# Kernel tuning notes

Hardware: AMD Instinct MI355X
Metric: run time of the kernel (lower is better)

Reference implementation:

```python
import jax, jax.numpy as jnp
import numpy as np

N_USER = 100000
N_ITEM = 50000
N = N_USER + N_ITEM
N_EDGES = 1200000
D = 64
NEG_SLOPE = 0.01  # torch leaky_relu default
EPS = 1e-12       # torch F.normalize default


def setup_inputs() -> dict:
    key = jax.random.key(0)
    ks = jax.random.split(key, 9)
    user_emb = jax.random.normal(ks[0], (N_USER, D), dtype=jnp.float32) * 0.1
    item_emb = jax.random.normal(ks[1], (N_ITEM, D), dtype=jnp.float32) * 0.1
    edge_row = jax.random.randint(ks[2], (N_EDGES,), 0, N, dtype=jnp.int32)
    edge_col = jax.random.randint(ks[3], (N_EDGES,), 0, N, dtype=jnp.int32)
    edge_val = jax.random.uniform(ks[4], (N_EDGES,), dtype=jnp.float32)
    Wf = jax.random.normal(ks[5], (3, D, D), dtype=jnp.float32) * (1.0 / np.sqrt(D))
    bf = jnp.zeros((3, D), dtype=jnp.float32)
    Wb = jax.random.normal(ks[6], (3, D, D), dtype=jnp.float32) * (1.0 / np.sqrt(D))
    bb = jnp.zeros((3, D), dtype=jnp.float32)
    return {"user_emb": user_emb, "item_emb": item_emb,
            "edge_row": edge_row, "edge_col": edge_col, "edge_val": edge_val,
            "Wf": Wf, "bf": bf, "Wb": Wb, "bb": bb}


def _spmm_plus_eye(edge_row, edge_col, edge_val, E):
    # (H + I) @ E : gather source features, scale, segment-sum into rows, add E
    msgs = edge_val[:, None] * E[edge_col]          # [n_edges, D]
    agg = jax.ops.segment_sum(msgs, edge_row, num_segments=N)
    return agg + E


def reference(user_emb, item_emb, edge_row, edge_col, edge_val, Wf, bf, Wb, bb):
    E_l = jnp.concatenate([user_emb, item_emb], axis=0)  # [N, D]
    all_emb = [E_l]
    for i in range(3):
        front = _spmm_plus_eye(edge_row, edge_col, edge_val, E_l)
        front_cal = jax.nn.leaky_relu(front @ Wf[i].T + bf[i], NEG_SLOPE)
        back = jax.nn.leaky_relu((E_l * front) @ Wb[i].T + bb[i], NEG_SLOPE)
        E_l = front_cal + back  # dropout p=0.5 treated as eval-mode identity
        norm = jnp.maximum(jnp.linalg.norm(E_l, axis=1, keepdims=True), EPS)
        all_emb.append(E_l / norm)
    all_emb = jnp.concatenate(all_emb, axis=1)  # [N, 4*D]
    return all_emb[:N_USER], all_emb[N_USER:]
```

## Files before the change

kernel.cpp:

```cpp
#include <hip/hip_runtime.h>
#include <hip/hip_bf16.h>
#include <stdint.h>

#define N_USER 100000
#define N_ITEM 50000
#define NTOT   150000
#define NEDGE  1200000
#define D      64
#define OUTD   256
#define NEG    0.01f
#define NBLK   586
#define LSTR   65

typedef __attribute__((ext_vector_type(8))) short short8;
typedef __attribute__((ext_vector_type(4))) float f32x4;

__device__ inline ushort f2bf(float x) {
    uint32_t u = __float_as_uint(x);
    u += 0x7fffu + ((u >> 16) & 1u);
    return (ushort)(u >> 16);
}
__device__ inline void split2(float x, ushort& h, ushort& l) {
    ushort hh = f2bf(x);
    float hf = __uint_as_float(((uint32_t)hh) << 16);
    h = hh;
    l = f2bf(x - hf);
}
__device__ inline void split8(const float* p, short8& h8, short8& l8) {
    float4 v0 = *(const float4*)p;
    float4 v1 = *(const float4*)(p + 4);
    float vv[8] = {v0.x, v0.y, v0.z, v0.w, v1.x, v1.y, v1.z, v1.w};
    #pragma unroll
    for (int e = 0; e < 8; e++) {
        ushort h, l;
        split2(vv[e], h, l);
        h8[e] = (short)h; l8[e] = (short)l;
    }
}

__global__ void k_init(const float* __restrict__ ue, const float* __restrict__ ie,
                       float* __restrict__ E, float* __restrict__ out) {
    int t = blockIdx.x * blockDim.x + threadIdx.x;
    if (t >= NTOT * 16) return;
    int r = t >> 4, q = t & 15;
    const float* src = (r < N_USER) ? (ue + (size_t)r * D)
                                    : (ie + (size_t)(r - N_USER) * D);
    float4 v = *(const float4*)(src + q * 4);
    *(float4*)(E + (size_t)r * D + q * 4) = v;
    *(float4*)(out + (size_t)r * OUTD + q * 4) = v;
}

__global__ void k_hist(const int* __restrict__ row, int* __restrict__ cnt) {
    int e = blockIdx.x * blockDim.x + threadIdx.x;
    if (e < NEDGE) atomicAdd(&cnt[row[e]], 1);
}

__global__ void k_scan_a(const int* __restrict__ cnt, int* __restrict__ part) {
    __shared__ int s[4];
    int i = blockIdx.x * 256 + threadIdx.x;
    int v = (i < NTOT) ? cnt[i] : 0;
    for (int off = 32; off; off >>= 1) v += __shfl_down(v, off, 64);
    if ((threadIdx.x & 63) == 0) s[threadIdx.x >> 6] = v;
    __syncthreads();
    if (threadIdx.x == 0) part[blockIdx.x] = s[0] + s[1] + s[2] + s[3];
}

__global__ void k_scan_b(int* __restrict__ part) {
    __shared__ int s[1024];
    int t = threadIdx.x;
    int v = (t < NBLK) ? part[t] : 0;
    s[t] = v;
    __syncthreads();
    for (int off = 1; off < 1024; off <<= 1) {
        int x = (t >= off) ? s[t - off] : 0;
        __syncthreads();
        s[t] += x;
        __syncthreads();
    }
    if (t < NBLK) part[t] = s[t] - v;
}

__global__ void k_scan_c(const int* __restrict__ cnt, const int* __restrict__ part,
                         int* __restrict__ offs, int* __restrict__ cur) {
    __shared__ int ws[4];
    int i = blockIdx.x * 256 + threadIdx.x;
    int v = (i < NTOT) ? cnt[i] : 0;
    int lane = threadIdx.x & 63, w = threadIdx.x >> 6;
    int x = v;
    for (int o = 1; o < 64; o <<= 1) {
        int y = __shfl_up(x, o, 64);
        if (lane >= o) x += y;
    }
    if (lane == 63) ws[w] = x;
    __syncthreads();
    int base = part[blockIdx.x];
    for (int k = 0; k < w; k++) base += ws[k];
    int excl = base + x - v;
    if (i < NTOT) { offs[i] = excl; cur[i] = excl; }
    if (i == 0) offs[NTOT] = NEDGE;
}

__global__ void k_scatter(const int* __restrict__ row, const int* __restrict__ col,
                          const float* __restrict__ val, int* __restrict__ cur,
                          int2* __restrict__ ce) {
    int e = blockIdx.x * blockDim.x + threadIdx.x;
    if (e >= NEDGE) return;
    int r = row[e];
    int p = atomicAdd(&cur[r], 1);
    int2 u;
    u.x = col[e];
    u.y = __float_as_int(val[e]);
    ce[p] = u;
}

__global__ void k_spmm(const float* __restrict__ E, const int* __restrict__ offs,
                       const int2* __restrict__ ce, float* __restrict__ front) {
    int r = blockIdx.x * (blockDim.x >> 6) + (threadIdx.x >> 6);
    int d = threadIdx.x & 63;
    if (r >= NTOT) return;
    int s = offs[r], e = offs[r + 1];
    float acc = E[(size_t)r * D + d];
    float a0 = 0.f, a1 = 0.f, a2 = 0.f, a3 = 0.f;
    int p = s;
    for (; p + 4 <= e; p += 4) {
        int2 c0 = ce[p + 0];
        int2 c1 = ce[p + 1];
        int2 c2 = ce[p + 2];
        int2 c3 = ce[p + 3];
        float x0 = E[(size_t)c0.x * D + d];
        float x1 = E[(size_t)c1.x * D + d];
        float x2 = E[(size_t)c2.x * D + d];
        float x3 = E[(size_t)c3.x * D + d];
        a0 = fmaf(__int_as_float(c0.y), x0, a0);
        a1 = fmaf(__int_as_float(c1.y), x1, a1);
        a2 = fmaf(__int_as_float(c2.y), x2, a2);
        a3 = fmaf(__int_as_float(c3.y), x3, a3);
    }
    for (; p < e; ++p) {
        int2 c = ce[p];
        acc = fmaf(__int_as_float(c.y), E[(size_t)c.x * D + d], acc);
    }
    acc += (a0 + a1) + (a2 + a3);
    front[(size_t)r * D + d] = acc;
}

__global__ __launch_bounds__(256) void k_rowmv(
    const float* __restrict__ front, float* __restrict__ E,
    const float* __restrict__ Wf, const float* __restrict__ bfv,
    const float* __restrict__ Wb, const float* __restrict__ bbv,
    float* __restrict__ out, int chunk) {
    __shared__ float sf[16 * LSTR];
    __shared__ float sg[16 * LSTR];
    __shared__ float nrm[16][4];

    int t  = threadIdx.x;
    int r0 = blockIdx.x * 16;

    {
        int row = t >> 4, km = (t & 15) * 4;
        const float* fp = front + (size_t)(r0 + row) * D + km;
        const float* ep = E     + (size_t)(r0 + row) * D + km;
        float4 a = *(const float4*)fp;
        float4 b = *(const float4*)ep;
        *(float4*)(sf + row * LSTR + km) = a;
        float4 gv;
        gv.x = a.x * b.x; gv.y = a.y * b.y; gv.z = a.z * b.z; gv.w = a.w * b.w;
        *(float4*)(sg + row * LSTR + km) = gv;
    }

    int lane = t & 63;
    int w    = t >> 6;
    int cl   = lane & 15;
    int kg   = lane >> 4;

    int col = w * 16 + cl;

    short8 wfh0, wfl0, wbh0, wbl0, wfh1, wfl1, wbh1, wbl1;
    split8(Wf + (size_t)col * D +  0 + kg * 8, wfh0, wfl0);
    split8(Wb + (size_t)col * D +  0 + kg * 8, wbh0, wbl0);
    split8(Wf + (size_t)col * D + 32 + kg * 8, wfh1, wfl1);
    split8(Wb + (size_t)col * D + 32 + kg * 8, wbh1, wbl1);
    float bF = bfv[col], bB = bbv[col];

    __syncthreads();

    f32x4 accF = {0.f, 0.f, 0.f, 0.f};
    f32x4 accB = {0.f, 0.f, 0.f, 0.f};
    {
        short8 fh, fl, gh, gl;
        split8(sf + cl * LSTR +  0 + kg * 8, fh, fl);
        split8(sg + cl * LSTR +  0 + kg * 8, gh, gl);
        accF = __builtin_amdgcn_mfma_f32_16x16x32_bf16(fh, wfh0, accF, 0, 0, 0);
        accB = __builtin_amdgcn_mfma_f32_16x16x32_bf16(gh, wbh0, accB, 0, 0, 0);
        accF = __builtin_amdgcn_mfma_f32_16x16x32_bf16(fl, wfh0, accF, 0, 0, 0);
        accB = __builtin_amdgcn_mfma_f32_16x16x32_bf16(gl, wbh0, accB, 0, 0, 0);
        accF = __builtin_amdgcn_mfma_f32_16x16x32_bf16(fh, wfl0, accF, 0, 0, 0);
        accB = __builtin_amdgcn_mfma_f32_16x16x32_bf16(gh, wbl0, accB, 0, 0, 0);
        split8(sf + cl * LSTR + 32 + kg * 8, fh, fl);
        split8(sg + cl * LSTR + 32 + kg * 8, gh, gl);
        accF = __builtin_amdgcn_mfma_f32_16x16x32_bf16(fh, wfh1, accF, 0, 0, 0);
        accB = __builtin_amdgcn_mfma_f32_16x16x32_bf16(gh, wbh1, accB, 0, 0, 0);
        accF = __builtin_amdgcn_mfma_f32_16x16x32_bf16(fl, wfh1, accF, 0, 0, 0);
        accB = __builtin_amdgcn_mfma_f32_16x16x32_bf16(gl, wbh1, accB, 0, 0, 0);
        accF = __builtin_amdgcn_mfma_f32_16x16x32_bf16(fh, wfl1, accF, 0, 0, 0);
        accB = __builtin_amdgcn_mfma_f32_16x16x32_bf16(gh, wbl1, accB, 0, 0, 0);
    }

    float e4[4], p4[4];
    #pragma unroll
    for (int rg = 0; rg < 4; rg++) {
        float aF = accF[rg] + bF;
        float aB = accB[rg] + bB;
        float vF = (aF > 0.f) ? aF : NEG * aF;
        float vB = (aB > 0.f) ? aB : NEG * aB;
        float e = vF + vB;
        e4[rg] = e;
        float p = e * e;
        p += __shfl_xor(p, 1, 64);
        p += __shfl_xor(p, 2, 64);
        p += __shfl_xor(p, 4, 64);
        p += __shfl_xor(p, 8, 64);
        p4[rg] = p;
    }
    if (cl == 0) {
        #pragma unroll
        for (int rg = 0; rg < 4; rg++) nrm[kg * 4 + rg][w] = p4[rg];
    }
    __syncthreads();
    #pragma unroll
    for (int rg = 0; rg < 4; rg++) {
        int row = kg * 4 + rg;
        float4 nv = *(const float4*)&nrm[row][0];
        float nsq = (nv.x + nv.y) + (nv.z + nv.w);
        float inv = 1.0f / fmaxf(sqrtf(nsq), 1e-12f);
        E[(size_t)(r0 + row) * D + col] = e4[rg];
        out[(size_t)(r0 + row) * OUTD + (size_t)chunk * D + col] = e4[rg] * inv;
    }
}

extern "C" void kernel_launch(void* const* d_in, const int* in_sizes, int n_in,
                              void* d_out, int out_size, void* d_ws, size_t ws_size,
                              hipStream_t stream) {
    const float* ue   = (const float*)d_in[0];
    const float* ie   = (const float*)d_in[1];
    const int*   erow = (const int*)d_in[2];
    const int*   ecol = (const int*)d_in[3];
    const float* eval = (const float*)d_in[4];
    const float* Wf   = (const float*)d_in[5];
    const float* bfv  = (const float*)d_in[6];
    const float* Wb   = (const float*)d_in[7];
    const float* bbv  = (const float*)d_in[8];
    float* out = (float*)d_out;

    float* E     = (float*)d_ws;
    float* front = E + (size_t)NTOT * D;
    float* invn  = front + (size_t)NTOT * D;
    int*   cnt   = (int*)(invn + NTOT);
    int*   offs  = cnt + NTOT;
    int*   cur   = offs + NTOT + 1;
    int*   part  = cur + NTOT;
    int2*  ce    = (int2*)(part + 1024);

    hipMemsetAsync(cnt, 0, NTOT * sizeof(int), stream);
    k_init<<<(NTOT * 16 + 255) / 256, 256, 0, stream>>>(ue, ie, E, out);
    k_hist<<<(NEDGE + 255) / 256, 256, 0, stream>>>(erow, cnt);
    k_scan_a<<<NBLK, 256, 0, stream>>>(cnt, part);
    k_scan_b<<<1, 1024, 0, stream>>>(part);
    k_scan_c<<<NBLK, 256, 0, stream>>>(cnt, part, offs, cur);
    k_scatter<<<(NEDGE + 255) / 256, 256, 0, stream>>>(erow, ecol, eval, cur, ce);

    for (int i = 0; i < 3; i++) {
        k_spmm<<<(NTOT + 3) / 4, 256, 0, stream>>>(E, offs, ce, front);
        k_rowmv<<<NTOT / 16, 256, 0, stream>>>(
            front, E, Wf + (size_t)i * D * D, bfv + (size_t)i * D,
            Wb + (size_t)i * D * D, bbv + (size_t)i * D, out, i + 1);
    }
}
```

Baseline: 700.7 us.

## Fuse SpMM into per-layer dense kernel with ping-pong E buffers

The separate SpMM and row-matmul kernels are merged into one per-layer kernel. Each block gathers neighbor rows for its 16 rows, with 16 lanes per row loading float4 chunks, and writes front and E*front straight into shared memory, so the front buffer no longer round-trips through global memory. E is double-buffered so one layer can read the old embeddings while writing the new ones, and the init and histogram kernels are merged into one launch. The trade-off is less parallelism in the gather: 16 threads per row instead of 64, with float4 loads, and 16 rows per block share one load-imbalance profile.

```diff
diff --git a/kernel.cpp b/kernel.cpp
--- a/kernel.cpp
+++ b/kernel.cpp
@@ -11,6 +11,7 @@
 #define NEG    0.01f
 #define NBLK   586
 #define LSTR   65
+#define INITBLK 9375
 
 typedef __attribute__((ext_vector_type(8))) short short8;
 typedef __attribute__((ext_vector_type(4))) float f32x4;
@@ -38,21 +39,21 @@
     }
 }
 
-__global__ void k_init(const float* __restrict__ ue, const float* __restrict__ ie,
-                       float* __restrict__ E, float* __restrict__ out) {
-    int t = blockIdx.x * blockDim.x + threadIdx.x;
-    if (t >= NTOT * 16) return;
-    int r = t >> 4, q = t & 15;
-    const float* src = (r < N_USER) ? (ue + (size_t)r * D)
-                                    : (ie + (size_t)(r - N_USER) * D);
-    float4 v = *(const float4*)(src + q * 4);
-    *(float4*)(E + (size_t)r * D + q * 4) = v;
-    *(float4*)(out + (size_t)r * OUTD + q * 4) = v;
-}
-
-__global__ void k_hist(const int* __restrict__ row, int* __restrict__ cnt) {
-    int e = blockIdx.x * blockDim.x + threadIdx.x;
-    if (e < NEDGE) atomicAdd(&cnt[row[e]], 1);
+__global__ void k_init_hist(const float* __restrict__ ue, const float* __restrict__ ie,
+                            float* __restrict__ E, float* __restrict__ out,
+                            const int* __restrict__ row, int* __restrict__ cnt) {
+    if (blockIdx.x < INITBLK) {
+        int t = blockIdx.x * 256 + threadIdx.x;
+        int r = t >> 4, q = t & 15;
+        const float* src = (r < N_USER) ? (ue + (size_t)r * D)
+                                        : (ie + (size_t)(r - N_USER) * D);
+        float4 v = *(const float4*)(src + q * 4);
+        *(float4*)(E + (size_t)r * D + q * 4) = v;
+        *(float4*)(out + (size_t)r * OUTD + q * 4) = v;
+    } else {
+        int e = (blockIdx.x - INITBLK) * 256 + threadIdx.x;
+        if (e < NEDGE) atomicAdd(&cnt[row[e]], 1);
+    }
 }
 
 __global__ void k_scan_a(const int* __restrict__ cnt, int* __restrict__ part) {
@@ -113,39 +114,9 @@
     ce[p] = u;
 }
 
-__global__ void k_spmm(const float* __restrict__ E, const int* __restrict__ offs,
-                       const int2* __restrict__ ce, float* __restrict__ front) {
-    int r = blockIdx.x * (blockDim.x >> 6) + (threadIdx.x >> 6);
-    int d = threadIdx.x & 63;
-    if (r >= NTOT) return;
-    int s = offs[r], e = offs[r + 1];
-    float acc = E[(size_t)r * D + d];
-    float a0 = 0.f, a1 = 0.f, a2 = 0.f, a3 = 0.f;
-    int p = s;
-    for (; p + 4 <= e; p += 4) {
-        int2 c0 = ce[p + 0];
-        int2 c1 = ce[p + 1];
-        int2 c2 = ce[p + 2];
-        int2 c3 = ce[p + 3];
-        float x0 = E[(size_t)c0.x * D + d];
-        float x1 = E[(size_t)c1.x * D + d];
-        float x2 = E[(size_t)c2.x * D + d];
-        float x3 = E[(size_t)c3.x * D + d];
-        a0 = fmaf(__int_as_float(c0.y), x0, a0);
-        a1 = fmaf(__int_as_float(c1.y), x1, a1);
-        a2 = fmaf(__int_as_float(c2.y), x2, a2);
-        a3 = fmaf(__int_as_float(c3.y), x3, a3);
-    }
-    for (; p < e; ++p) {
-        int2 c = ce[p];
-        acc = fmaf(__int_as_float(c.y), E[(size_t)c.x * D + d], acc);
-    }
-    acc += (a0 + a1) + (a2 + a3);
-    front[(size_t)r * D + d] = acc;
-}
-
-__global__ __launch_bounds__(256) void k_rowmv(
-    const float* __restrict__ front, float* __restrict__ E,
+__global__ __launch_bounds__(256) void k_layer(
+    const float* __restrict__ Ecur, float* __restrict__ Enx,
+    const int* __restrict__ offs, const int2* __restrict__ ce,
     const float* __restrict__ Wf, const float* __restrict__ bfv,
     const float* __restrict__ Wb, const float* __restrict__ bbv,
     float* __restrict__ out, int chunk) {
@@ -153,28 +124,14 @@
     __shared__ float sg[16 * LSTR];
     __shared__ float nrm[16][4];
 
-    int t  = threadIdx.x;
-    int r0 = blockIdx.x * 16;
-
-    {
-        int row = t >> 4, km = (t & 15) * 4;
-        const float* fp = front + (size_t)(r0 + row) * D + km;
-        const float* ep = E     + (size_t)(r0 + row) * D + km;
-        float4 a = *(const float4*)fp;
-        float4 b = *(const float4*)ep;
-        *(float4*)(sf + row * LSTR + km) = a;
-        float4 gv;
-        gv.x = a.x * b.x; gv.y = a.y * b.y; gv.z = a.z * b.z; gv.w = a.w * b.w;
-        *(float4*)(sg + row * LSTR + km) = gv;
-    }
-
+    int t    = threadIdx.x;
     int lane = t & 63;
     int w    = t >> 6;
     int cl   = lane & 15;
     int kg   = lane >> 4;
+    int r0   = blockIdx.x * 16;
 
     int col = w * 16 + cl;
-
     short8 wfh0, wfl0, wbh0, wbl0, wfh1, wfl1, wbh1, wbl1;
     split8(Wf + (size_t)col * D +  0 + kg * 8, wfh0, wfl0);
     split8(Wb + (size_t)col * D +  0 + kg * 8, wbh0, wbl0);
@@ -182,6 +139,53 @@
     split8(Wb + (size_t)col * D + 32 + kg * 8, wbh1, wbl1);
     float bF = bfv[col], bB = bbv[col];
 
+    {
+        int row = w * 4 + kg;
+        int d4  = cl * 4;
+        int r   = r0 + row;
+        float4 ei = *(const float4*)(Ecur + (size_t)r * D + d4);
+        float4 a0 = ei;
+        float4 a1 = {0.f,0.f,0.f,0.f}, a2 = {0.f,0.f,0.f,0.f}, a3 = {0.f,0.f,0.f,0.f};
+        int s = offs[r], e = offs[r + 1];
+        int p = s;
+        for (; p + 4 <= e; p += 4) {
+            int2 c0 = ce[p + 0];
+            int2 c1 = ce[p + 1];
+            int2 c2 = ce[p + 2];
+            int2 c3 = ce[p + 3];
+            float4 x0 = *(const float4*)(Ecur + (size_t)c0.x * D + d4);
+            float4 x1 = *(const float4*)(Ecur + (size_t)c1.x * D + d4);
+            float4 x2 = *(const float4*)(Ecur + (size_t)c2.x * D + d4);
+            float4 x3 = *(const float4*)(Ecur + (size_t)c3.x * D + d4);
+            float v0 = __int_as_float(c0.y), v1 = __int_as_float(c1.y);
+            float v2 = __int_as_float(c2.y), v3 = __int_as_float(c3.y);
+            a0.x = fmaf(v0, x0.x, a0.x); a0.y = fmaf(v0, x0.y, a0.y);
+            a0.z = fmaf(v0, x0.z, a0.z); a0.w = fmaf(v0, x0.w, a0.w);
+            a1.x = fmaf(v1, x1.x, a1.x); a1.y = fmaf(v1, x1.y, a1.y);
+            a1.z = fmaf(v1, x1.z, a1.z); a1.w = fmaf(v1, x1.w, a1.w);
+            a2.x = fmaf(v2, x2.x, a2.x); a2.y = fmaf(v2, x2.y, a2.y);
+            a2.z = fmaf(v2, x2.z, a2.z); a2.w = fmaf(v2, x2.w, a2.w);
+            a3.x = fmaf(v3, x3.x, a3.x); a3.y = fmaf(v3, x3.y, a3.y);
+            a3.z = fmaf(v3, x3.z, a3.z); a3.w = fmaf(v3, x3.w, a3.w);
+        }
+        for (; p < e; ++p) {
+            int2 c = ce[p];
+            float v = __int_as_float(c.y);
+            float4 x = *(const float4*)(Ecur + (size_t)c.x * D + d4);
+            a0.x = fmaf(v, x.x, a0.x); a0.y = fmaf(v, x.y, a0.y);
+            a0.z = fmaf(v, x.z, a0.z); a0.w = fmaf(v, x.w, a0.w);
+        }
+        float4 fr;
+        fr.x = (a0.x + a1.x) + (a2.x + a3.x);
+        fr.y = (a0.y + a1.y) + (a2.y + a3.y);
+        fr.z = (a0.z + a1.z) + (a2.z + a3.z);
+        fr.w = (a0.w + a1.w) + (a2.w + a3.w);
+        float4 gv;
+        gv.x = fr.x * ei.x; gv.y = fr.y * ei.y;
+        gv.z = fr.z * ei.z; gv.w = fr.w * ei.w;
+        *(float4*)(sf + row * LSTR + d4) = fr;
+        *(float4*)(sg + row * LSTR + d4) = gv;
+    }
     __syncthreads();
 
     f32x4 accF = {0.f, 0.f, 0.f, 0.f};
@@ -233,7 +237,7 @@
         float4 nv = *(const float4*)&nrm[row][0];
         float nsq = (nv.x + nv.y) + (nv.z + nv.w);
         float inv = 1.0f / fmaxf(sqrtf(nsq), 1e-12f);
-        E[(size_t)(r0 + row) * D + col] = e4[rg];
+        Enx[(size_t)(r0 + row) * D + col] = e4[rg];
         out[(size_t)(r0 + row) * OUTD + (size_t)chunk * D + col] = e4[rg] * inv;
     }
 }
@@ -252,27 +256,27 @@
     const float* bbv  = (const float*)d_in[8];
     float* out = (float*)d_out;
 
-    float* E     = (float*)d_ws;
-    float* front = E + (size_t)NTOT * D;
-    float* invn  = front + (size_t)NTOT * D;
-    int*   cnt   = (int*)(invn + NTOT);
-    int*   offs  = cnt + NTOT;
-    int*   cur   = offs + NTOT + 1;
-    int*   part  = cur + NTOT;
-    int2*  ce    = (int2*)(part + 1024);
+    float* E0   = (float*)d_ws;
+    float* E1   = E0 + (size_t)NTOT * D;
+    int*   cnt  = (int*)(E1 + (size_t)NTOT * D);
+    int*   offs = cnt + NTOT;
+    int*   cur  = offs + NTOT + 1;
+    int*   part = cur + NTOT;
+    int2*  ce   = (int2*)(part + 1024);
 
     hipMemsetAsync(cnt, 0, NTOT * sizeof(int), stream);
-    k_init<<<(NTOT * 16 + 255) / 256, 256, 0, stream>>>(ue, ie, E, out);
-    k_hist<<<(NEDGE + 255) / 256, 256, 0, stream>>>(erow, cnt);
+    k_init_hist<<<INITBLK + (NEDGE + 255) / 256, 256, 0, stream>>>(ue, ie, E0, out, erow, cnt);
     k_scan_a<<<NBLK, 256, 0, stream>>>(cnt, part);
     k_scan_b<<<1, 1024, 0, stream>>>(part);
     k_scan_c<<<NBLK, 256, 0, stream>>>(cnt, part, offs, cur);
     k_scatter<<<(NEDGE + 255) / 256, 256, 0, stream>>>(erow, ecol, eval, cur, ce);
 
+    const float* rd[3] = {E0, E1, E0};
+    float*       wr[3] = {E1, E0, E1};
     for (int i = 0; i < 3; i++) {
-        k_spmm<<<(NTOT + 3) / 4, 256, 0, stream>>>(E, offs, ce, front);
-        k_rowmv<<<NTOT / 16, 256, 0, stream>>>(
-            front, E, Wf + (size_t)i * D * D, bfv + (size_t)i * D,
+        k_layer<<<NTOT / 16, 256, 0, stream>>>(
+            rd[i], wr[i], offs, ce,
+            Wf + (size_t)i * D * D, bfv + (size_t)i * D,
             Wb + (size_t)i * D * D, bbv + (size_t)i * D, out, i + 1);
     }
 }
```

After: 730.4 us. +4.2%, slower.
